# Performance work log

Hardware: AMD Instinct MI355X
Metric: run time of the kernel (lower is better)

Reference implementation:

```python
import jax, jax.numpy as jnp
import numpy as np

B, R, C, O, I = 512, 1152, 10, 16, 8

def setup_inputs() -> dict:
    key = jax.random.key(0)
    k1, k2, k3 = jax.random.split(key, 3)
    std = np.sqrt(3.0 / (I * O)).astype(np.float32)
    x = jax.random.normal(k1, (B, R, I), dtype=jnp.float32)
    W = jax.random.normal(k2, (1, R, C, O, I), dtype=jnp.float32) * std
    bias = jax.random.normal(k3, (O, 1), dtype=jnp.float32) * std
    return {"x": x, "W": W, "bias": bias}

def reference(x, W, bias):
    # Original materializes x stacked over capsules and W tiled over batch;
    # mathematically this is a broadcasted batched matvec:
    # u_hat[b,r,c,o] = sum_i W[0,r,c,o,i] * x[b,r,i] + bias[o,0]
    u_hat = jnp.einsum('rcoi,bri->brco', W[0], x) + bias[:, 0]
    return u_hat[..., None]  # [B, R, C, O, 1] to match torch output shape
```

## Files before the change

### kernel.cpp

```cpp
#include <hip/hip_runtime.h>


#define B_ 512
#define R_ 1152
#define C_ 10
#define O_ 16
#define I_ 8
#define CO_ 160
#define SLOTS 40
#define GROUPS 8
#define NTHREADS (GROUPS * SLOTS)
#define BATCH_PER_BLOCK 256

__global__ __launch_bounds__(NTHREADS) void digitcaps_kernel(
    const float* __restrict__ x,
    const float* __restrict__ W,
    const float* __restrict__ bias,
    float* __restrict__ out)
{
    const int r = blockIdx.x;
    const int t = threadIdx.x;
    const int g = t / SLOTS;
    const int s = t - g * SLOTS;

    const float4* wp = (const float4*)(W + ((size_t)r * CO_ + (size_t)s * 4) * I_);
    float w[4][8];
#pragma unroll
    for (int j = 0; j < 4; ++j) {
        float4 lo = wp[2 * j];
        float4 hi = wp[2 * j + 1];
        w[j][0] = lo.x; w[j][1] = lo.y; w[j][2] = lo.z; w[j][3] = lo.w;
        w[j][4] = hi.x; w[j][5] = hi.y; w[j][6] = hi.z; w[j][7] = hi.w;
    }

    float4 bv = ((const float4*)bias)[s & 3];
    float bsf[4] = {bv.x, bv.y, bv.z, bv.w};

    const int b0 = blockIdx.y * BATCH_PER_BLOCK + g;
    const float* xp = x + ((size_t)b0 * R_ + r) * I_;
    float*       op = out + ((size_t)b0 * R_ + r) * CO_ + (size_t)s * 4;

    for (int it = 0; it < BATCH_PER_BLOCK / GROUPS; ++it) {
        float4 xlo = ((const float4*)xp)[0];
        float4 xhi = ((const float4*)xp)[1];
        float xf[8] = {xlo.x, xlo.y, xlo.z, xlo.w, xhi.x, xhi.y, xhi.z, xhi.w};

        float acc[4];
#pragma unroll
        for (int j = 0; j < 4; ++j) acc[j] = bsf[j];
#pragma unroll
        for (int i = 0; i < 8; ++i)
#pragma unroll
            for (int j = 0; j < 4; ++j)
                acc[j] = fmaf(xf[i], w[j][i], acc[j]);

        float4 ov = {acc[0], acc[1], acc[2], acc[3]};
        *(float4*)op = ov;

        xp += (size_t)GROUPS * R_ * I_;
        op += (size_t)GROUPS * R_ * CO_;
    }
}

extern "C" void kernel_launch(void* const* d_in, const int* in_sizes, int n_in,
                              void* d_out, int out_size, void* d_ws, size_t ws_size,
                              hipStream_t stream) {
    const float* x    = (const float*)d_in[0];
    const float* W    = (const float*)d_in[1];
    const float* bias = (const float*)d_in[2];
    float* out        = (float*)d_out;

    dim3 grid(R_, B_ / BATCH_PER_BLOCK);
    digitcaps_kernel<<<grid, NTHREADS, 0, stream>>>(x, W, bias, out);
}
```

Before: 441.1 us.

## Remap blocks to contiguous capsule rows per batch and use nontemporal stores

Each block now covers 8 consecutive input capsules for a slice of 16 batch elements, so every iteration writes one contiguous 5 KB span of output and reads contiguous x. Output stores become nontemporal to avoid polluting cache with the large streaming result. The cost is that W is reloaded per batch slice, 32 times instead of 2, relying on L2 for reuse.

New measurement: 428.7 us, median of 2. -2.8%, faster.

```diff
diff --git a/kernel.cpp b/kernel.cpp
--- a/kernel.cpp
+++ b/kernel.cpp
@@ -8,9 +8,11 @@
 #define I_ 8
 #define CO_ 160
 #define SLOTS 40
-#define GROUPS 8
-#define NTHREADS (GROUPS * SLOTS)
-#define BATCH_PER_BLOCK 256
+#define RPB 8
+#define NTHREADS (RPB * SLOTS)
+#define NB 16
+
+typedef float f32x4 __attribute__((ext_vector_type(4)));
 
 __global__ __launch_bounds__(NTHREADS) void digitcaps_kernel(
     const float* __restrict__ x,
@@ -18,31 +20,32 @@
     const float* __restrict__ bias,
     float* __restrict__ out)
 {
-    const int r = blockIdx.x;
-    const int t = threadIdx.x;
-    const int g = t / SLOTS;
-    const int s = t - g * SLOTS;
+    const int t  = threadIdx.x;
+    const int rr = t / SLOTS;
+    const int s  = t - rr * SLOTS;
+    const int r  = blockIdx.x * RPB + rr;
 
-    const float4* wp = (const float4*)(W + ((size_t)r * CO_ + (size_t)s * 4) * I_);
+    const f32x4* wp = (const f32x4*)(W + ((size_t)r * CO_ + (size_t)s * 4) * I_);
     float w[4][8];
 #pragma unroll
     for (int j = 0; j < 4; ++j) {
-        float4 lo = wp[2 * j];
-        float4 hi = wp[2 * j + 1];
+        f32x4 lo = wp[2 * j];
+        f32x4 hi = wp[2 * j + 1];
         w[j][0] = lo.x; w[j][1] = lo.y; w[j][2] = lo.z; w[j][3] = lo.w;
         w[j][4] = hi.x; w[j][5] = hi.y; w[j][6] = hi.z; w[j][7] = hi.w;
     }
 
-    float4 bv = ((const float4*)bias)[s & 3];
+    f32x4 bv = ((const f32x4*)bias)[s & 3];
     float bsf[4] = {bv.x, bv.y, bv.z, bv.w};
 
-    const int b0 = blockIdx.y * BATCH_PER_BLOCK + g;
+    const int b0 = blockIdx.y * NB;
     const float* xp = x + ((size_t)b0 * R_ + r) * I_;
     float*       op = out + ((size_t)b0 * R_ + r) * CO_ + (size_t)s * 4;
 
-    for (int it = 0; it < BATCH_PER_BLOCK / GROUPS; ++it) {
-        float4 xlo = ((const float4*)xp)[0];
-        float4 xhi = ((const float4*)xp)[1];
+#pragma unroll 4
+    for (int bb = 0; bb < NB; ++bb) {
+        f32x4 xlo = ((const f32x4*)xp)[0];
+        f32x4 xhi = ((const f32x4*)xp)[1];
         float xf[8] = {xlo.x, xlo.y, xlo.z, xlo.w, xhi.x, xhi.y, xhi.z, xhi.w};
 
         float acc[4];
@@ -54,11 +57,11 @@
             for (int j = 0; j < 4; ++j)
                 acc[j] = fmaf(xf[i], w[j][i], acc[j]);
 
-        float4 ov = {acc[0], acc[1], acc[2], acc[3]};
-        *(float4*)op = ov;
+        f32x4 ov = {acc[0], acc[1], acc[2], acc[3]};
+        __builtin_nontemporal_store(ov, (f32x4*)op);
 
-        xp += (size_t)GROUPS * R_ * I_;
-        op += (size_t)GROUPS * R_ * CO_;
+        xp += (size_t)R_ * I_;
+        op += (size_t)R_ * CO_;
     }
 }
 
@@ -70,6 +73,6 @@
     const float* bias = (const float*)d_in[2];
     float* out        = (float*)d_out;
 
-    dim3 grid(R_, B_ / BATCH_PER_BLOCK);
+    dim3 grid(R_ / RPB, B_ / NB);
     digitcaps_kernel<<<grid, NTHREADS, 0, stream>>>(x, W, bias, out);
 }
```
